# Optimization experiments

Hardware: AMD Instinct MI355X
Metric: run time of the kernel (lower is better)

Reference implementation:

```python
import jax, jax.numpy as jnp
import numpy as np

T, B, E, H = 2048, 4, 1024, 16
HD = E // H
SCALE = HD ** -0.5


def setup_inputs() -> dict:
    key = jax.random.key(0)
    k1, k2, k3 = jax.random.split(key, 3)
    # xavier-ish scaling on weights for numerical sanity
    inputs = jax.random.normal(k1, (T, B, E), dtype=jnp.float32)
    in_proj_weight = jax.random.normal(k2, (3 * E, E), dtype=jnp.float32) * (2.0 / (4 * E)) ** 0.5
    out_proj_weight = jax.random.normal(k3, (E, E), dtype=jnp.float32) * (1.0 / E) ** 0.5
    return {"inputs": inputs, "in_proj_weight": in_proj_weight, "out_proj_weight": out_proj_weight}


def reference(inputs, in_proj_weight, out_proj_weight):
    t, b, e = inputs.shape
    # fused QKV projection: [T,B,E] @ [E,3E] -> [T, B*H, 3, HD]
    qkv = jnp.einsum('tbe,fe->tbf', inputs, in_proj_weight)
    qkv = qkv.reshape(t, b * H, 3, HD)
    q, k, v = qkv[:, :, 0, :], qkv[:, :, 1, :], qkv[:, :, 2, :]  # [T, B*H, HD]
    # scaled attention scores per (batch*head): [B*H, T, T]
    scores = SCALE * jnp.einsum('tnd,snd->nts', q, k)
    probs = jax.nn.softmax(scores, axis=-1)
    # dropout p=0.0 -> identity
    ctx = jnp.einsum('nts,snd->tnd', probs, v).reshape(t, b, e)
    # output projection (applied to attention context, matching intended math / backward)
    return jnp.einsum('tbe,oe->tbo', ctx, out_proj_weight)
```

## Files before the change

### kernel.cpp

```cpp
#include <hip/hip_runtime.h>
#include <stdint.h>
#include <stddef.h>


typedef __attribute__((ext_vector_type(8))) short bf16x8;
typedef __attribute__((ext_vector_type(4))) short bf16x4;
typedef __attribute__((ext_vector_type(4))) float f32x4;
typedef __attribute__((ext_vector_type(4))) unsigned int u32x4;
typedef __attribute__((ext_vector_type(2))) unsigned int u32x2;

#define MFMA16(a, b, c) __builtin_amdgcn_mfma_f32_16x16x32_bf16((a), (b), (c), 0, 0, 0)

#if __has_builtin(__builtin_amdgcn_mfma_f32_16x16x16bf16_1k)
#define HAVE_K16 1
#define MFMAK16(a, b, c) __builtin_amdgcn_mfma_f32_16x16x16bf16_1k((a), (b), (c), 0, 0, 0)
#endif

__device__ __forceinline__ unsigned short f2bf(float f) {
  unsigned u = __builtin_bit_cast(unsigned, f);
  u += 0x7fffu + ((u >> 16) & 1u);
  return (unsigned short)(u >> 16);
}

__device__ __forceinline__ float fast_exp2(float x) {
#if __has_builtin(__builtin_amdgcn_exp2f)
  return __builtin_amdgcn_exp2f(x);
#else
  return exp2f(x);
#endif
}

__device__ __forceinline__ unsigned cvtpk(float lo, float hi) {
  unsigned r;
  asm volatile("v_cvt_pk_bf16_f32 %0, %1, %2" : "=v"(r) : "v"(lo), "v"(hi));
  return r;
}

#ifndef HAVE_K16
__device__ __forceinline__ void lane_swap32(unsigned &a, unsigned &b) {
#if __has_builtin(__builtin_amdgcn_permlane32_swap)
  auto r = __builtin_amdgcn_permlane32_swap(a, b, false, false);
  a = r[0]; b = r[1];
#else
  const bool hi = (threadIdx.x & 32) != 0;
  unsigned sa = (unsigned)__shfl_xor((int)a, 32, 64);
  unsigned sb = (unsigned)__shfl_xor((int)b, 32, 64);
  unsigned na = hi ? sb : a;
  unsigned nb = hi ? b : sa;
  a = na; b = nb;
#endif
}
__device__ __forceinline__ void lane_swap16(unsigned &a, unsigned &b) {
  const bool odd = (threadIdx.x & 16) != 0;
  unsigned sa = (unsigned)__shfl_xor((int)a, 16, 64);
  unsigned sb = (unsigned)__shfl_xor((int)b, 16, 64);
  unsigned na = odd ? sb : a;
  unsigned nb = odd ? b : sa;
  a = na; b = nb;
}
#endif

__device__ __forceinline__ void gload_lds16(const void* g, void* l) {
  __builtin_amdgcn_global_load_lds((const __attribute__((address_space(1))) void*)g,
                                   (__attribute__((address_space(3))) void*)l,
                                   16, 0, 0);
}

__global__ __launch_bounds__(256) void k_cvt(const float* __restrict__ src,
                                             unsigned short* __restrict__ dst, int n4) {
  int i = blockIdx.x * 256 + threadIdx.x;
  if (i >= n4) return;
  const float4 v = ((const float4*)src)[i];
  ushort4 o;
  o.x = f2bf(v.x); o.y = f2bf(v.y); o.z = f2bf(v.z); o.w = f2bf(v.w);
  ((ushort4*)dst)[i] = o;
}

__global__ __launch_bounds__(256, 2) void k_gemm_qkv(
    const unsigned short* __restrict__ A,
    const unsigned short* __restrict__ Bt,
    unsigned short* __restrict__ Qb,
    unsigned short* __restrict__ Kb,
    unsigned short* __restrict__ Vb) {
  constexpr int K = 1024;
  __shared__ __align__(16) unsigned short As[128 * 32];
  __shared__ __align__(16) unsigned short Bs[128 * 32];
  const int tid = threadIdx.x;
  const int l = tid & 63, w = tid >> 6;
  const int lr = l & 15, lg = l >> 4;
  const int bm = blockIdx.x, bn = blockIdx.y;
  const int wr = (w >> 1) * 64, wc = (w & 1) * 64;

  f32x4 acc[4][4] = {};

  const int o0 = tid * 16, o1 = tid * 16 + 4096;
  const int r0 = o0 >> 6, c0 = o0 & 63;
  const int r1 = o1 >> 6, c1 = o1 & 63;
  const char* gA0 = (const char*)A + (size_t)(bm * 128 + r0) * (K * 2) + c0;
  const char* gA1 = (const char*)A + (size_t)(bm * 128 + r1) * (K * 2) + c1;
  const char* gB0 = (const char*)Bt + (size_t)(bn * 128 + r0) * (K * 2) + c0;
  const char* gB1 = (const char*)Bt + (size_t)(bn * 128 + r1) * (K * 2) + c1;
  char* lA0 = (char*)As + o0;
  char* lA1 = (char*)As + o1;
  char* lB0 = (char*)Bs + o0;
  char* lB1 = (char*)Bs + o1;

  for (int kt = 0; kt < K / 32; ++kt) {
    const int kb = kt * 64;
    gload_lds16(gA0 + kb, lA0);
    gload_lds16(gA1 + kb, lA1);
    gload_lds16(gB0 + kb, lB0);
    gload_lds16(gB1 + kb, lB1);
    __syncthreads();
    bf16x8 af[4], bfr[4];
#pragma unroll
    for (int mf = 0; mf < 4; ++mf)
      af[mf] = *(const bf16x8*)&As[(wr + mf * 16 + lr) * 32 + lg * 8];
#pragma unroll
    for (int nf = 0; nf < 4; ++nf)
      bfr[nf] = *(const bf16x8*)&Bs[(wc + nf * 16 + lr) * 32 + lg * 8];
#pragma unroll
    for (int mf = 0; mf < 4; ++mf)
#pragma unroll
      for (int nf = 0; nf < 4; ++nf)
        acc[mf][nf] = MFMA16(af[mf], bfr[nf], acc[mf][nf]);
    __syncthreads();
  }

#pragma unroll
  for (int nf = 0; nf < 4; ++nf) {
    const int f = bn * 128 + wc + nf * 16 + lr;
    const int hq = f / 192;
    const int s3 = (f >> 6) % 3;
    const int d = f & 63;
    unsigned short* dst = (s3 == 0) ? Qb : (s3 == 1) ? Kb : Vb;
    const float qscale = (s3 == 0) ? 0.18033688011112042f : 1.0f;
#pragma unroll
    for (int mf = 0; mf < 4; ++mf) {
#pragma unroll
      for (int i = 0; i < 4; ++i) {
        const int r = bm * 128 + wr + mf * 16 + lg * 4 + i;
        const int t = r >> 2, bb2 = r & 3;
        const int nIdx = bb2 * 16 + hq;
        dst[((size_t)nIdx * 2048 + t) * 64 + d] = f2bf(acc[mf][nf][i] * qscale);
      }
    }
  }
}

__global__ __launch_bounds__(256) void k_vtrans(const unsigned short* __restrict__ V,
                                                unsigned short* __restrict__ VT) {
  __shared__ unsigned short tile[64][66];
  const int tid = threadIdx.x;
  const int n = blockIdx.y, t0 = blockIdx.x * 64;
  const int r = tid >> 2, c0 = (tid & 3) * 16;
  const unsigned short* src = V + ((size_t)(n * 2048 + t0 + r) * 64 + c0);
  bf16x8 a = *(const bf16x8*)src;
  bf16x8 b = *(const bf16x8*)(src + 8);
#pragma unroll
  for (int j = 0; j < 8; ++j) tile[r][c0 + j] = (unsigned short)a[j];
#pragma unroll
  for (int j = 0; j < 8; ++j) tile[r][c0 + 8 + j] = (unsigned short)b[j];
  __syncthreads();
  const int d = tid >> 2, u0 = (tid & 3) * 16;
  bf16x8 oA, oB;
#pragma unroll
  for (int j = 0; j < 8; ++j) oA[j] = (short)tile[u0 + j][d];
#pragma unroll
  for (int j = 0; j < 8; ++j) oB[j] = (short)tile[u0 + 8 + j][d];
  unsigned short* dst = VT + ((size_t)(n * 64 + d) * 2048 + t0 + u0);
  *(bf16x8*)dst = oA;
  *(bf16x8*)(dst + 8) = oB;
}

__global__ __launch_bounds__(256, 2) void k_attn(
    const unsigned short* __restrict__ Qb, const unsigned short* __restrict__ Kb,
    const unsigned short* __restrict__ VTb, unsigned short* __restrict__ Cx) {
  __shared__ __align__(16) unsigned short Ks[2][64 * 64];
  __shared__ __align__(16) unsigned short Vt[2][64 * 64];

  const int tid = threadIdx.x;
  const int l = tid & 63, w = tid >> 6;
  const int lq = l & 15, lg = l >> 4;
  const int n = blockIdx.x, qt = blockIdx.y;

  const unsigned short* Qh = Qb + (size_t)n * (2048 * 64);
  const unsigned short* Kh = Kb + (size_t)n * (2048 * 64);
  const unsigned short* Vh = VTb + (size_t)n * (64 * 2048);

  bf16x8 aq[2][2];
#pragma unroll
  for (int qf = 0; qf < 2; ++qf)
#pragma unroll
    for (int kd = 0; kd < 2; ++kd)
      aq[qf][kd] = *(const bf16x8*)&Qh[(size_t)(qt * 128 + w * 32 + qf * 16 + lq) * 64 +
                                       kd * 32 + lg * 8];

  f32x4 o[4][2] = {};
  float lsum[2] = {0.f, 0.f};

  char* Ksl = (char*)&Ks[0][0];
  char* Vtl = (char*)&Vt[0][0];

  auto STAGE = [&](int buf, int st) {
    const int s0 = st * 64;
#pragma unroll
    for (int it = 0; it < 2; ++it) {
      const int off = (it * 256 + tid) * 16;
      const int row = off >> 7;
      const int colb = (off & 127) ^ ((row & 7) << 4);
      gload_lds16((const char*)Kh + ((size_t)(s0 + row) << 7) + colb, Ksl + buf * 8192 + off);
      gload_lds16((const char*)Vh + ((size_t)row << 12) + (s0 << 1) + colb, Vtl + buf * 8192 + off);
    }
  };

  STAGE(0, 0);
  asm volatile("s_waitcnt vmcnt(0)" ::: "memory");
  __builtin_amdgcn_s_barrier();

#pragma unroll 2
  for (int st = 0; st < 32; ++st) {
    const int cur = st & 1;
    if (st + 1 < 32) STAGE(cur ^ 1, st + 1);

    const char* Kc = Ksl + cur * 8192;
    const char* Vc = Vtl + cur * 8192;

    f32x4 sc[2][4];
    __builtin_amdgcn_s_setprio(1);
#pragma unroll
    for (int sf = 0; sf < 4; ++sf) {
      const int rowk = sf * 16 + lq;
      const int sw = (rowk & 7) << 4;
      bf16x8 k0 = *(const bf16x8*)(Kc + ((rowk * 128 + lg * 16) ^ sw));
      bf16x8 k1 = *(const bf16x8*)(Kc + ((rowk * 128 + 64 + lg * 16) ^ sw));
#pragma unroll
      for (int qf = 0; qf < 2; ++qf) {
        f32x4 z = {0.f, 0.f, 0.f, 0.f};
        z = MFMA16(k0, aq[qf][0], z);
        z = MFMA16(k1, aq[qf][1], z);
        sc[qf][sf] = z;
      }
    }
    __builtin_amdgcn_s_setprio(0);

#pragma unroll
    for (int qf = 0; qf < 2; ++qf) {
      float accs = 0.f;
#pragma unroll
      for (int sf = 0; sf < 4; ++sf)
#pragma unroll
        for (int i = 0; i < 4; ++i) {
          const float p = fast_exp2(sc[qf][sf][i]);
          sc[qf][sf][i] = p;
          accs += p;
        }
      lsum[qf] += accs;
    }

    __builtin_amdgcn_s_setprio(1);
#ifdef HAVE_K16
#pragma unroll
    for (int sf = 0; sf < 4; ++sf) {
      bf16x4 pf[2];
#pragma unroll
      for (int qf = 0; qf < 2; ++qf) {
        u32x2 pu = {cvtpk(sc[qf][sf][0], sc[qf][sf][1]),
                    cvtpk(sc[qf][sf][2], sc[qf][sf][3])};
        pf[qf] = __builtin_bit_cast(bf16x4, pu);
      }
#pragma unroll
      for (int df = 0; df < 4; ++df) {
        const int rowd = df * 16 + lq;
        const int sw = (rowd & 7) << 4;
        bf16x4 vf = *(const bf16x4*)(Vc + ((rowd * 128 + sf * 32 + lg * 8) ^ sw));
        o[df][0] = MFMAK16(vf, pf[0], o[df][0]);
        o[df][1] = MFMAK16(vf, pf[1], o[df][1]);
      }
    }
#else
#pragma unroll
    for (int kb = 0; kb < 2; ++kb) {
      bf16x8 pf[2];
#pragma unroll
      for (int qf = 0; qf < 2; ++qf) {
        unsigned w0 = cvtpk(sc[qf][2 * kb + 0][0], sc[qf][2 * kb + 0][1]);
        unsigned w1 = cvtpk(sc[qf][2 * kb + 0][2], sc[qf][2 * kb + 0][3]);
        unsigned w2 = cvtpk(sc[qf][2 * kb + 1][0], sc[qf][2 * kb + 1][1]);
        unsigned w3 = cvtpk(sc[qf][2 * kb + 1][2], sc[qf][2 * kb + 1][3]);
        lane_swap32(w0, w2);
        lane_swap32(w1, w3);
        lane_swap16(w0, w2);
        lane_swap16(w1, w3);
        u32x4 t4 = {w0, w1, w2, w3};
        pf[qf] = __builtin_bit_cast(bf16x8, t4);
      }
#pragma unroll
      for (int df = 0; df < 4; ++df) {
        const int rowd = df * 16 + lq;
        const int sw = (rowd & 7) << 4;
        bf16x8 vf = *(const bf16x8*)(Vc + ((rowd * 128 + kb * 64 + lg * 16) ^ sw));
#pragma unroll
        for (int qf = 0; qf < 2; ++qf)
          o[df][qf] = MFMA16(vf, pf[qf], o[df][qf]);
      }
    }
#endif
    __builtin_amdgcn_s_setprio(0);

    asm volatile("s_waitcnt vmcnt(0)" ::: "memory");
    __builtin_amdgcn_s_barrier();
  }

  const int bb = n >> 4, h = n & 15;
#pragma unroll
  for (int qf = 0; qf < 2; ++qf) {
    float li = lsum[qf];
    li += __shfl_xor(li, 16, 64);
    li += __shfl_xor(li, 32, 64);
    const float inv = 1.0f / li;
    const int q = qt * 128 + w * 32 + qf * 16 + lq;
#pragma unroll
    for (int df = 0; df < 4; ++df) {
      ushort4 pk;
      pk.x = f2bf(o[df][qf][0] * inv);
      pk.y = f2bf(o[df][qf][1] * inv);
      pk.z = f2bf(o[df][qf][2] * inv);
      pk.w = f2bf(o[df][qf][3] * inv);
      *(ushort4*)&Cx[(size_t)(q * 4 + bb) * 1024 + h * 64 + df * 16 + lg * 4] = pk;
    }
  }
}

__global__ __launch_bounds__(256, 2) void k_gemm_out(
    const unsigned short* __restrict__ A,
    const unsigned short* __restrict__ Bt,
    float* __restrict__ C) {
  constexpr int K = 1024;
  __shared__ __align__(16) unsigned short As[128 * 32];
  __shared__ __align__(16) unsigned short Bs[128 * 32];
  const int tid = threadIdx.x;
  const int l = tid & 63, w = tid >> 6;
  const int lr = l & 15, lg = l >> 4;
  const int bm = blockIdx.x, bn = blockIdx.y;
  const int wr = (w >> 1) * 64, wc = (w & 1) * 64;

  f32x4 acc[4][4] = {};

  const int o0 = tid * 16, o1 = tid * 16 + 4096;
  const int r0 = o0 >> 6, c0 = o0 & 63;
  const int r1 = o1 >> 6, c1 = o1 & 63;
  const char* gA0 = (const char*)A + (size_t)(bm * 128 + r0) * (K * 2) + c0;
  const char* gA1 = (const char*)A + (size_t)(bm * 128 + r1) * (K * 2) + c1;
  const char* gB0 = (const char*)Bt + (size_t)(bn * 128 + r0) * (K * 2) + c0;
  const char* gB1 = (const char*)Bt + (size_t)(bn * 128 + r1) * (K * 2) + c1;
  char* lA0 = (char*)As + o0;
  char* lA1 = (char*)As + o1;
  char* lB0 = (char*)Bs + o0;
  char* lB1 = (char*)Bs + o1;

  for (int kt = 0; kt < K / 32; ++kt) {
    const int kb = kt * 64;
    gload_lds16(gA0 + kb, lA0);
    gload_lds16(gA1 + kb, lA1);
    gload_lds16(gB0 + kb, lB0);
    gload_lds16(gB1 + kb, lB1);
    __syncthreads();
    bf16x8 af[4], bfr[4];
#pragma unroll
    for (int mf = 0; mf < 4; ++mf)
      af[mf] = *(const bf16x8*)&As[(wr + mf * 16 + lr) * 32 + lg * 8];
#pragma unroll
    for (int nf = 0; nf < 4; ++nf)
      bfr[nf] = *(const bf16x8*)&Bs[(wc + nf * 16 + lr) * 32 + lg * 8];
#pragma unroll
    for (int mf = 0; mf < 4; ++mf)
#pragma unroll
      for (int nf = 0; nf < 4; ++nf)
        acc[mf][nf] = MFMA16(af[mf], bfr[nf], acc[mf][nf]);
    __syncthreads();
  }

#pragma unroll
  for (int mf = 0; mf < 4; ++mf)
#pragma unroll
    for (int i = 0; i < 4; ++i) {
      const int r = bm * 128 + wr + mf * 16 + lg * 4 + i;
#pragma unroll
      for (int nf = 0; nf < 4; ++nf)
        C[(size_t)r * 1024 + bn * 128 + wc + nf * 16 + lr] = acc[mf][nf][i];
    }
}

extern "C" void kernel_launch(void* const* d_in, const int* in_sizes, int n_in,
                              void* d_out, int out_size, void* d_ws, size_t ws_size,
                              hipStream_t stream) {
  const float* X = (const float*)d_in[0];
  const float* W1 = (const float*)d_in[1];
  const float* Wo = (const float*)d_in[2];
  float* out = (float*)d_out;

  char* ws = (char*)d_ws;
  unsigned short* Xb  = (unsigned short*)(ws);
  unsigned short* W1b = (unsigned short*)(ws + 16777216);
  unsigned short* Wob = (unsigned short*)(ws + 23068672);
  unsigned short* Qb  = (unsigned short*)(ws + 25165824);
  unsigned short* Kb  = (unsigned short*)(ws + 41943040);
  unsigned short* VTb = (unsigned short*)(ws + 58720256);
  unsigned short* Vb  = (unsigned short*)(ws + 75497472);
  unsigned short* Cx  = (unsigned short*)(ws + 75497472);

  k_cvt<<<8192, 256, 0, stream>>>(X, Xb, 2097152);
  k_cvt<<<3072, 256, 0, stream>>>(W1, W1b, 786432);
  k_cvt<<<1024, 256, 0, stream>>>(Wo, Wob, 262144);
  k_gemm_qkv<<<dim3(64, 24), 256, 0, stream>>>(Xb, W1b, Qb, Kb, Vb);
  k_vtrans<<<dim3(32, 64), 256, 0, stream>>>(Vb, VTb);
  k_attn<<<dim3(64, 16), 256, 0, stream>>>(Qb, Kb, VTb, Cx);
  k_gemm_out<<<dim3(64, 8), 256, 0, stream>>>(Cx, Wob, out);
}
```

Baseline: 212.1 us.

## Double attention query tile per block and interleave QK, softmax and PV per half-tile

Each attention block now handles 256 queries (64 per wave) instead of 128, halving the grid so each staged K/V tile is reused by twice as many query rows. The score, exp and PV steps are restructured to run per 32-key half of the tile, which keeps live score registers bounded, and the K16 MFMA path is dropped in favour of the 16x16x32 path with lane swaps. permlane16_swap is used when available. The cost is more accumulator registers per wave, which can lower occupancy, and only 512 blocks to spread across the CUs.

```diff
diff --git a/kernel.cpp b/kernel.cpp
--- a/kernel.cpp
+++ b/kernel.cpp
@@ -4,17 +4,10 @@
 
 
 typedef __attribute__((ext_vector_type(8))) short bf16x8;
-typedef __attribute__((ext_vector_type(4))) short bf16x4;
 typedef __attribute__((ext_vector_type(4))) float f32x4;
 typedef __attribute__((ext_vector_type(4))) unsigned int u32x4;
-typedef __attribute__((ext_vector_type(2))) unsigned int u32x2;
 
 #define MFMA16(a, b, c) __builtin_amdgcn_mfma_f32_16x16x32_bf16((a), (b), (c), 0, 0, 0)
-
-#if __has_builtin(__builtin_amdgcn_mfma_f32_16x16x16bf16_1k)
-#define HAVE_K16 1
-#define MFMAK16(a, b, c) __builtin_amdgcn_mfma_f32_16x16x16bf16_1k((a), (b), (c), 0, 0, 0)
-#endif
 
 __device__ __forceinline__ unsigned short f2bf(float f) {
   unsigned u = __builtin_bit_cast(unsigned, f);
@@ -36,7 +29,6 @@
   return r;
 }
 
-#ifndef HAVE_K16
 __device__ __forceinline__ void lane_swap32(unsigned &a, unsigned &b) {
 #if __has_builtin(__builtin_amdgcn_permlane32_swap)
   auto r = __builtin_amdgcn_permlane32_swap(a, b, false, false);
@@ -50,15 +42,20 @@
   a = na; b = nb;
 #endif
 }
+
 __device__ __forceinline__ void lane_swap16(unsigned &a, unsigned &b) {
+#if __has_builtin(__builtin_amdgcn_permlane16_swap)
+  auto r = __builtin_amdgcn_permlane16_swap(a, b, false, false);
+  a = r[0]; b = r[1];
+#else
   const bool odd = (threadIdx.x & 16) != 0;
   unsigned sa = (unsigned)__shfl_xor((int)a, 16, 64);
   unsigned sb = (unsigned)__shfl_xor((int)b, 16, 64);
   unsigned na = odd ? sb : a;
   unsigned nb = odd ? b : sa;
   a = na; b = nb;
-}
 #endif
+}
 
 __device__ __forceinline__ void gload_lds16(const void* g, void* l) {
   __builtin_amdgcn_global_load_lds((const __attribute__((address_space(1))) void*)g,
@@ -188,16 +185,16 @@
   const unsigned short* Kh = Kb + (size_t)n * (2048 * 64);
   const unsigned short* Vh = VTb + (size_t)n * (64 * 2048);
 
-  bf16x8 aq[2][2];
-#pragma unroll
-  for (int qf = 0; qf < 2; ++qf)
+  bf16x8 aq[4][2];
+#pragma unroll
+  for (int qf = 0; qf < 4; ++qf)
 #pragma unroll
     for (int kd = 0; kd < 2; ++kd)
-      aq[qf][kd] = *(const bf16x8*)&Qh[(size_t)(qt * 128 + w * 32 + qf * 16 + lq) * 64 +
+      aq[qf][kd] = *(const bf16x8*)&Qh[(size_t)(qt * 256 + w * 64 + qf * 16 + lq) * 64 +
                                        kd * 32 + lg * 8];
 
-  f32x4 o[4][2] = {};
-  float lsum[2] = {0.f, 0.f};
+  f32x4 o[4][4] = {};
+  float lsum[4] = {0.f, 0.f, 0.f, 0.f};
 
   char* Ksl = (char*)&Ks[0][0];
   char* Vtl = (char*)&Vt[0][0];
@@ -226,86 +223,57 @@
     const char* Kc = Ksl + cur * 8192;
     const char* Vc = Vtl + cur * 8192;
 
-    f32x4 sc[2][4];
     __builtin_amdgcn_s_setprio(1);
 #pragma unroll
-    for (int sf = 0; sf < 4; ++sf) {
-      const int rowk = sf * 16 + lq;
-      const int sw = (rowk & 7) << 4;
-      bf16x8 k0 = *(const bf16x8*)(Kc + ((rowk * 128 + lg * 16) ^ sw));
-      bf16x8 k1 = *(const bf16x8*)(Kc + ((rowk * 128 + 64 + lg * 16) ^ sw));
-#pragma unroll
-      for (int qf = 0; qf < 2; ++qf) {
-        f32x4 z = {0.f, 0.f, 0.f, 0.f};
-        z = MFMA16(k0, aq[qf][0], z);
-        z = MFMA16(k1, aq[qf][1], z);
-        sc[qf][sf] = z;
+    for (int kb = 0; kb < 2; ++kb) {
+      bf16x8 kf[2][2];
+#pragma unroll
+      for (int sfl = 0; sfl < 2; ++sfl) {
+        const int rowk = (2 * kb + sfl) * 16 + lq;
+        const int sw = (rowk & 7) << 4;
+        kf[sfl][0] = *(const bf16x8*)(Kc + ((rowk * 128 + lg * 16) ^ sw));
+        kf[sfl][1] = *(const bf16x8*)(Kc + ((rowk * 128 + 64 + lg * 16) ^ sw));
       }
-    }
-    __builtin_amdgcn_s_setprio(0);
-
-#pragma unroll
-    for (int qf = 0; qf < 2; ++qf) {
-      float accs = 0.f;
-#pragma unroll
-      for (int sf = 0; sf < 4; ++sf)
+
+      bf16x8 pq[4];
+#pragma unroll
+      for (int qf = 0; qf < 4; ++qf) {
+        f32x4 s0 = {0.f, 0.f, 0.f, 0.f};
+        f32x4 s1 = {0.f, 0.f, 0.f, 0.f};
+        s0 = MFMA16(kf[0][0], aq[qf][0], s0);
+        s0 = MFMA16(kf[0][1], aq[qf][1], s0);
+        s1 = MFMA16(kf[1][0], aq[qf][0], s1);
+        s1 = MFMA16(kf[1][1], aq[qf][1], s1);
+        float accs = 0.f;
 #pragma unroll
         for (int i = 0; i < 4; ++i) {
-          const float p = fast_exp2(sc[qf][sf][i]);
-          sc[qf][sf][i] = p;
-          accs += p;
+          s0[i] = fast_exp2(s0[i]);
+          s1[i] = fast_exp2(s1[i]);
+          accs += s0[i] + s1[i];
         }
-      lsum[qf] += accs;
-    }
-
-    __builtin_amdgcn_s_setprio(1);
-#ifdef HAVE_K16
-#pragma unroll
-    for (int sf = 0; sf < 4; ++sf) {
-      bf16x4 pf[2];
-#pragma unroll
-      for (int qf = 0; qf < 2; ++qf) {
-        u32x2 pu = {cvtpk(sc[qf][sf][0], sc[qf][sf][1]),
-                    cvtpk(sc[qf][sf][2], sc[qf][sf][3])};
-        pf[qf] = __builtin_bit_cast(bf16x4, pu);
-      }
-#pragma unroll
-      for (int df = 0; df < 4; ++df) {
-        const int rowd = df * 16 + lq;
-        const int sw = (rowd & 7) << 4;
-        bf16x4 vf = *(const bf16x4*)(Vc + ((rowd * 128 + sf * 32 + lg * 8) ^ sw));
-        o[df][0] = MFMAK16(vf, pf[0], o[df][0]);
-        o[df][1] = MFMAK16(vf, pf[1], o[df][1]);
-      }
-    }
-#else
-#pragma unroll
-    for (int kb = 0; kb < 2; ++kb) {
-      bf16x8 pf[2];
-#pragma unroll
-      for (int qf = 0; qf < 2; ++qf) {
-        unsigned w0 = cvtpk(sc[qf][2 * kb + 0][0], sc[qf][2 * kb + 0][1]);
-        unsigned w1 = cvtpk(sc[qf][2 * kb + 0][2], sc[qf][2 * kb + 0][3]);
-        unsigned w2 = cvtpk(sc[qf][2 * kb + 1][0], sc[qf][2 * kb + 1][1]);
-        unsigned w3 = cvtpk(sc[qf][2 * kb + 1][2], sc[qf][2 * kb + 1][3]);
+        lsum[qf] += accs;
+        unsigned w0 = cvtpk(s0[0], s0[1]);
+        unsigned w1 = cvtpk(s0[2], s0[3]);
+        unsigned w2 = cvtpk(s1[0], s1[1]);
+        unsigned w3 = cvtpk(s1[2], s1[3]);
         lane_swap32(w0, w2);
         lane_swap32(w1, w3);
         lane_swap16(w0, w2);
         lane_swap16(w1, w3);
         u32x4 t4 = {w0, w1, w2, w3};
-        pf[qf] = __builtin_bit_cast(bf16x8, t4);
+        pq[qf] = __builtin_bit_cast(bf16x8, t4);
       }
+
 #pragma unroll
       for (int df = 0; df < 4; ++df) {
         const int rowd = df * 16 + lq;
         const int sw = (rowd & 7) << 4;
         bf16x8 vf = *(const bf16x8*)(Vc + ((rowd * 128 + kb * 64 + lg * 16) ^ sw));
 #pragma unroll
-        for (int qf = 0; qf < 2; ++qf)
-          o[df][qf] = MFMA16(vf, pf[qf], o[df][qf]);
+        for (int qf = 0; qf < 4; ++qf)
+          o[df][qf] = MFMA16(vf, pq[qf], o[df][qf]);
       }
     }
-#endif
     __builtin_amdgcn_s_setprio(0);
 
     asm volatile("s_waitcnt vmcnt(0)" ::: "memory");
@@ -314,12 +282,12 @@
 
   const int bb = n >> 4, h = n & 15;
 #pragma unroll
-  for (int qf = 0; qf < 2; ++qf) {
+  for (int qf = 0; qf < 4; ++qf) {
     float li = lsum[qf];
     li += __shfl_xor(li, 16, 64);
     li += __shfl_xor(li, 32, 64);
     const float inv = 1.0f / li;
-    const int q = qt * 128 + w * 32 + qf * 16 + lq;
+    const int q = qt * 256 + w * 64 + qf * 16 + lq;
 #pragma unroll
     for (int df = 0; df < 4; ++df) {
       ushort4 pk;
@@ -415,6 +383,6 @@
   k_cvt<<<1024, 256, 0, stream>>>(Wo, Wob, 262144);
   k_gemm_qkv<<<dim3(64, 24), 256, 0, stream>>>(Xb, W1b, Qb, Kb, Vb);
   k_vtrans<<<dim3(32, 64), 256, 0, stream>>>(Vb, VTb);
-  k_attn<<<dim3(64, 16), 256, 0, stream>>>(Qb, Kb, VTb, Cx);
+  k_attn<<<dim3(64, 8), 256, 0, stream>>>(Qb, Kb, VTb, Cx);
   k_gemm_out<<<dim3(64, 8), 256, 0, stream>>>(Cx, Wob, out);
 }
```

Result: faster. 197.9 us (-6.7%).
